# Performance work log

Hardware: AMD Instinct MI355X
Metric: run time of the kernel (lower is better)

## Reference

```python
import jax, jax.numpy as jnp
import numpy as np
from jax import lax

KSIZE = 7
EPS = 1e-10


def _circular_mask(k=KSIZE):
    # faithful to EdgeLoss.cal_mask: inclusive circle, normalized by count
    xs = np.arange(k, dtype=np.float32)
    d2 = (xs[:, None] + 0.5 - k / 2) ** 2 + (xs[None, :] + 0.5 - k / 2) ** 2
    m = (d2 <= ((k - 1) / 2) ** 2).astype(np.float32)
    return jnp.asarray(m / m.sum())


def _gather_logp(prob, target):
    # prob: (B,C,H,W), target: (B,H,W) int -> log prob at target class, (B,1,H,W)
    logpt = jnp.log(prob + EPS)
    return jnp.take_along_axis(logpt, target[:, None, :, :], axis=1)


def _focal0(prob, target):
    # FocalLoss(gamma=0, alpha=None): mean of -log p_t
    return jnp.mean(-_gather_logp(prob, target))


def _dice(prob, target):
    t = target.astype(prob.dtype)          # (B,H,W)
    p = prob[:, 1, :, :]                   # foreground channel
    I = jnp.sum(p * t, axis=(1, 2))
    U = jnp.sum(p + t, axis=(1, 2))
    return 1.0 - jnp.mean(2.0 * I / (U + EPS))


def _edge(prob, target, mask):
    # circular box-filter average of target == unfold+mask sum (zero padding)
    t = target.astype(prob.dtype)[:, None, :, :]  # (B,1,H,W)
    ave = lax.conv_general_dilated(t, mask[None, None, :, :], (1, 1), 'SAME')
    at = jnp.abs(t - ave)                          # edge weight (B,1,H,W)
    lp = _gather_logp(prob, target)                # (B,1,H,W)
    return jnp.mean(-lp * at)


def _calloss(prob, target, sigmas, mask):
    return (_focal0(prob, target) / sigmas[0]
            + _dice(prob, target) / sigmas[1]
            + _edge(prob, target, mask) / sigmas[2])


def setup_inputs() -> dict:
    key = jax.random.key(0)
    k1, k2, k3, k4, k5 = jax.random.split(key, 5)
    N, M, B, C, H, W = 2, 1, 8, 2, 1024, 1024
    predictions = jax.random.normal(k1, (N, B, C, H, W), dtype=jnp.float32)
    Diss = jax.random.uniform(k2, (M, B, C, H, W), dtype=jnp.float32)
    target = jax.random.randint(k3, (B, H, W), 0, 2, dtype=jnp.int32)
    diff = jax.random.normal(k4, (), dtype=jnp.float32)
    sigma = jax.random.uniform(k5, (3,), dtype=jnp.float32, minval=0.5, maxval=1.5)
    return {"predictions": predictions, "Diss": Diss, "target": target,
            "diff": diff, "sigma": sigma}


def reference(predictions, Diss, target, diff, sigma):
    mask = _circular_mask()
    sigmas = sigma * sigma
    loss = jnp.asarray(0.0, dtype=predictions.dtype)
    for i in range(predictions.shape[0]):            # deep-supervision heads
        prob = jax.nn.softmax(predictions[i], axis=1)
        loss = loss + _calloss(prob, target, sigmas, mask)
    for j in range(Diss.shape[0]):                   # already-probabilities
        loss = loss + _calloss(Diss[j], target, sigmas, mask)
    loss = loss + diff                               # len(diff) != 0 branch
    loss = loss + jnp.sum(jnp.log(sigmas)) / 2
    return loss
```

## Files before the change

kernel.cpp:

```cpp
#include <hip/hip_runtime.h>
#include <math.h>

#define BB 8
#define HH 1024
#define WW 1024
#define HW (1024*1024)

#define TW 128
#define TH 16
#define HALO_H (TH+6)
#define TSTRIDE 136
#define NCOPY 32
#define NSLOT 18

__global__ __launch_bounds__(256)
void loss_main(const float* __restrict__ pred,
               const float* __restrict__ diss,
               const int*   __restrict__ target,
               double*      __restrict__ acc)
{
    __shared__ float tile[HALO_H][TSTRIDE];
    __shared__ float h5[HALO_H][TW];
    __shared__ float h7[HALO_H][TW];
    __shared__ float red[4][12];

    const int bx = blockIdx.x;
    const int by = blockIdx.y;
    const int b  = blockIdx.z;
    const int x0 = bx * TW, y0 = by * TH;
    const int tid = threadIdx.x;
    const int txx = tid & 31;
    const int ty  = tid >> 5;

    const int* tgt_b = target + (size_t)b * HW;
    for (int ch = tid; ch < HALO_H * 34; ch += 256) {
        int r = ch / 34;
        int m = ch - r * 34;
        int gy  = y0 - 3 + r;
        int gxb = x0 - 4 + 4 * m;
        float4 v = make_float4(0.f, 0.f, 0.f, 0.f);
        if (gy >= 0 && gy < HH) {
            if (gxb >= 0 && gxb + 3 < WW) {
                const int4 iv = *(const int4*)(tgt_b + (size_t)gy * WW + gxb);
                v.x = (float)iv.x; v.y = (float)iv.y;
                v.z = (float)iv.z; v.w = (float)iv.w;
            } else {
                #pragma unroll
                for (int j = 0; j < 4; ++j) {
                    int gx = gxb + j;
                    ((float*)&v)[j] = (gx >= 0 && gx < WW)
                        ? (float)tgt_b[(size_t)gy * WW + gx] : 0.f;
                }
            }
        }
        *(float4*)&tile[r][4 * m] = v;
    }
    __syncthreads();

    for (int g = tid; g < HALO_H * 32; g += 256) {
        int r  = g >> 5;
        int xg = (g & 31) << 2;
        float4 c0 = *(const float4*)&tile[r][xg];
        float4 c1 = *(const float4*)&tile[r][xg + 4];
        float4 c2 = *(const float4*)&tile[r][xg + 8];
        float s1 = c0.y, s2 = c0.z, s3 = c0.w;
        float s4 = c1.x, s5 = c1.y, s6 = c1.z, s7 = c1.w;
        float s8 = c2.x, s9 = c2.y, s10 = c2.z;
        float4 v5, v7;
        v5.x = s2 + s3 + s4 + s5 + s6;
        v5.y = s3 + s4 + s5 + s6 + s7;
        v5.z = s4 + s5 + s6 + s7 + s8;
        v5.w = s5 + s6 + s7 + s8 + s9;
        v7.x = v5.x + s1 + s7;
        v7.y = v5.y + s2 + s8;
        v7.z = v5.z + s3 + s9;
        v7.w = v5.w + s4 + s10;
        *(float4*)&h5[r][xg] = v5;
        *(float4*)&h7[r][xg] = v7;
    }
    __syncthreads();

    const float* p00 = pred + ((size_t)(0 * BB + b) * 2 + 0) * HW;
    const float* p01 = p00 + HW;
    const float* p10 = pred + ((size_t)(1 * BB + b) * 2 + 0) * HW;
    const float* p11 = p10 + HW;
    const float* q0  = diss + ((size_t)b * 2 + 0) * HW;
    const float* q1  = q0 + HW;

    float sf0=0.f, se0=0.f, si0=0.f, su0=0.f;
    float sf1=0.f, se1=0.f, si1=0.f, su1=0.f;
    float sf2=0.f, se2=0.f, si2=0.f, su2=0.f;

    const int x  = txx * 4;
    const int gx = x0 + x;
    #pragma unroll
    for (int k = 0; k < 2; ++k) {
        const int r  = ty + 8 * k;
        const int gy = y0 + r;
        const size_t off = (size_t)gy * WW + gx;

        float4 t4  = *(const float4*)&tile[r + 3][x + 4];
        float4 top = *(const float4*)&tile[r    ][x + 4];
        float4 bot = *(const float4*)&tile[r + 6][x + 4];
        float4 a1v = *(const float4*)&h5[r + 1][x];
        float4 a2v = *(const float4*)&h5[r + 2][x];
        float4 a3v = *(const float4*)&h7[r + 3][x];
        float4 a4v = *(const float4*)&h5[r + 4][x];
        float4 a5v = *(const float4*)&h5[r + 5][x];

        float4 v00 = *(const float4*)(p00 + off);
        float4 v01 = *(const float4*)(p01 + off);
        float4 v10 = *(const float4*)(p10 + off);
        float4 v11 = *(const float4*)(p11 + off);
        float4 w0  = *(const float4*)(q0  + off);
        float4 w1  = *(const float4*)(q1  + off);

        float4 cnt;
        cnt.x = top.x + a1v.x + a2v.x + a3v.x + a4v.x + a5v.x + bot.x;
        cnt.y = top.y + a1v.y + a2v.y + a3v.y + a4v.y + a5v.y + bot.y;
        cnt.z = top.z + a1v.z + a2v.z + a3v.z + a4v.z + a5v.z + bot.z;
        cnt.w = top.w + a1v.w + a2v.w + a3v.w + a4v.w + a5v.w + bot.w;

        #pragma unroll
        for (int j = 0; j < 4; ++j) {
            const float t  = ((const float*)&t4)[j];
            const float at = fabsf(t - ((const float*)&cnt)[j] * (1.0f / 29.0f));
            {
                float a0 = ((const float*)&v00)[j], a1 = ((const float*)&v01)[j];
                float p1v = __builtin_amdgcn_rcpf(1.0f + __expf(a0 - a1));
                float pt  = (t != 0.0f) ? p1v : 1.0f - p1v;
                float lp  = __logf(pt + 1e-10f);
                sf0 -= lp; se0 -= lp * at; si0 += p1v * t; su0 += p1v + t;
            }
            {
                float a0 = ((const float*)&v10)[j], a1 = ((const float*)&v11)[j];
                float p1v = __builtin_amdgcn_rcpf(1.0f + __expf(a0 - a1));
                float pt  = (t != 0.0f) ? p1v : 1.0f - p1v;
                float lp  = __logf(pt + 1e-10f);
                sf1 -= lp; se1 -= lp * at; si1 += p1v * t; su1 += p1v + t;
            }
            {
                float d0 = ((const float*)&w0)[j], d1 = ((const float*)&w1)[j];
                float pt = (t != 0.0f) ? d1 : d0;
                float lp = __logf(pt + 1e-10f);
                sf2 -= lp; se2 -= lp * at; si2 += d1 * t; su2 += d1 + t;
            }
        }
    }

    float vals[12] = {sf0,se0,si0,su0, sf1,se1,si1,su1, sf2,se2,si2,su2};
    #pragma unroll
    for (int j = 0; j < 12; ++j) {
        float v = vals[j];
        #pragma unroll
        for (int s = 32; s > 0; s >>= 1) v += __shfl_down(v, s, 64);
        vals[j] = v;
    }
    const int wave = tid >> 6;
    const int lane = tid & 63;
    if (lane == 0) {
        #pragma unroll
        for (int j = 0; j < 12; ++j) red[wave][j] = vals[j];
    }
    __syncthreads();
    if (tid < 12) {
        double s = (double)red[0][tid] + (double)red[1][tid]
                 + (double)red[2][tid] + (double)red[3][tid];
        const int img  = tid >> 2;
        const int what = tid & 3;
        int slot;
        if      (what == 0) slot = 0;
        else if (what == 1) slot = 1;
        else if (what == 2) slot = 2 + b;
        else                slot = 10 + b;
        const int copy = (by * 8 + bx) & (NCOPY - 1);
        unsafeAtomicAdd(acc + ((size_t)(img * NSLOT + slot) * NCOPY + copy), s);
    }
}

__global__ __launch_bounds__(256)
void finalize_kernel(const double* __restrict__ acc,
                     const float*  __restrict__ diff,
                     const float*  __restrict__ sigma,
                     float*        __restrict__ out)
{
    __shared__ double ssum[54];
    const int t = threadIdx.x;
    if (t < 216) {
        const int slot_lin = t >> 2;
        const int part     = t & 3;
        const double* p = acc + (size_t)slot_lin * NCOPY + part * 8;
        double s = 0.0;
        #pragma unroll
        for (int j = 0; j < 8; ++j) s += p[j];
        s += __shfl_down(s, 1, 64);
        s += __shfl_down(s, 2, 64);
        if (part == 0) ssum[slot_lin] = s;
    }
    __syncthreads();
    if (t == 0) {
        const double sig0 = (double)sigma[0] * (double)sigma[0];
        const double sig1 = (double)sigma[1] * (double)sigma[1];
        const double sig2 = (double)sigma[2] * (double)sigma[2];
        const double inv  = 1.0 / (double)((size_t)BB * HW);
        double loss = 0.0;
        for (int i = 0; i < 3; ++i) {
            const double* A = ssum + i * NSLOT;
            double focal = A[0] * inv;
            double edge  = A[1] * inv;
            double dsum  = 0.0;
            for (int b = 0; b < BB; ++b)
                dsum += 2.0 * A[2 + b] / (A[10 + b] + 1e-10);
            double dice = 1.0 - dsum / (double)BB;
            loss += focal / sig0 + dice / sig1 + edge / sig2;
        }
        loss += (double)diff[0];
        loss += 0.5 * (log(sig0) + log(sig1) + log(sig2));
        out[0] = (float)loss;
    }
}

extern "C" void kernel_launch(void* const* d_in, const int* in_sizes, int n_in,
                              void* d_out, int out_size, void* d_ws, size_t ws_size,
                              hipStream_t stream)
{
    const float* pred   = (const float*)d_in[0];
    const float* diss   = (const float*)d_in[1];
    const int*   target = (const int*)  d_in[2];
    const float* diff   = (const float*)d_in[3];
    const float* sigma  = (const float*)d_in[4];
    double* acc = (double*)d_ws;

    hipMemsetAsync(d_ws, 0, (size_t)3 * NSLOT * NCOPY * sizeof(double), stream);

    dim3 grid(WW / TW, HH / TH, BB);
    loss_main<<<grid, 256, 0, stream>>>(pred, diss, target, acc);
    finalize_kernel<<<1, 256, 0, stream>>>(acc, diff, sigma, (float*)d_out);
}
```

Baseline: 270.6 us.

## Pack target tile into bytes and compute box sums with SWAR integer adds

Stores the target halo tile and horizontal partial sums as packed 8-bit lanes instead of floats. The 5- and 7-wide horizontal sums and the vertical accumulation then run as SIMD-within-a-register integer adds. This cuts shared memory roughly fourfold, allowing a higher occupancy hint (launch bounds of 8 blocks), and reduces LDS traffic and ALU work. It relies on the box count fitting in 8 bits (at most 29) and on target values being 0/1, and adds byte extraction and int-to-float conversions per pixel.

```diff
diff --git a/kernel.cpp b/kernel.cpp
--- a/kernel.cpp
+++ b/kernel.cpp
@@ -13,15 +13,15 @@
 #define NCOPY 32
 #define NSLOT 18
 
-__global__ __launch_bounds__(256)
+__global__ __launch_bounds__(256, 8)
 void loss_main(const float* __restrict__ pred,
                const float* __restrict__ diss,
                const int*   __restrict__ target,
                double*      __restrict__ acc)
 {
-    __shared__ float tile[HALO_H][TSTRIDE];
-    __shared__ float h5[HALO_H][TW];
-    __shared__ float h7[HALO_H][TW];
+    __shared__ __align__(16) unsigned char tile[HALO_H][TSTRIDE];
+    __shared__ __align__(16) unsigned char h5[HALO_H][TW];
+    __shared__ __align__(16) unsigned char h7[HALO_H][TW];
     __shared__ float red[4][12];
 
     const int bx = blockIdx.x;
@@ -38,45 +38,43 @@
         int m = ch - r * 34;
         int gy  = y0 - 3 + r;
         int gxb = x0 - 4 + 4 * m;
-        float4 v = make_float4(0.f, 0.f, 0.f, 0.f);
+        unsigned v = 0u;
         if (gy >= 0 && gy < HH) {
             if (gxb >= 0 && gxb + 3 < WW) {
                 const int4 iv = *(const int4*)(tgt_b + (size_t)gy * WW + gxb);
-                v.x = (float)iv.x; v.y = (float)iv.y;
-                v.z = (float)iv.z; v.w = (float)iv.w;
+                v = (unsigned)(iv.x & 0xff)
+                  | ((unsigned)(iv.y & 0xff) << 8)
+                  | ((unsigned)(iv.z & 0xff) << 16)
+                  | ((unsigned)(iv.w & 0xff) << 24);
             } else {
                 #pragma unroll
                 for (int j = 0; j < 4; ++j) {
                     int gx = gxb + j;
-                    ((float*)&v)[j] = (gx >= 0 && gx < WW)
-                        ? (float)tgt_b[(size_t)gy * WW + gx] : 0.f;
+                    if (gx >= 0 && gx < WW)
+                        v |= (unsigned)(tgt_b[(size_t)gy * WW + gx] & 0xff) << (8 * j);
                 }
             }
         }
-        *(float4*)&tile[r][4 * m] = v;
+        *(unsigned*)&tile[r][4 * m] = v;
     }
     __syncthreads();
 
     for (int g = tid; g < HALO_H * 32; g += 256) {
         int r  = g >> 5;
         int xg = (g & 31) << 2;
-        float4 c0 = *(const float4*)&tile[r][xg];
-        float4 c1 = *(const float4*)&tile[r][xg + 4];
-        float4 c2 = *(const float4*)&tile[r][xg + 8];
-        float s1 = c0.y, s2 = c0.z, s3 = c0.w;
-        float s4 = c1.x, s5 = c1.y, s6 = c1.z, s7 = c1.w;
-        float s8 = c2.x, s9 = c2.y, s10 = c2.z;
-        float4 v5, v7;
-        v5.x = s2 + s3 + s4 + s5 + s6;
-        v5.y = s3 + s4 + s5 + s6 + s7;
-        v5.z = s4 + s5 + s6 + s7 + s8;
-        v5.w = s5 + s6 + s7 + s8 + s9;
-        v7.x = v5.x + s1 + s7;
-        v7.y = v5.y + s2 + s8;
-        v7.z = v5.z + s3 + s9;
-        v7.w = v5.w + s4 + s10;
-        *(float4*)&h5[r][xg] = v5;
-        *(float4*)&h7[r][xg] = v7;
+        unsigned c0 = *(const unsigned*)&tile[r][xg];
+        unsigned c1 = *(const unsigned*)&tile[r][xg + 4];
+        unsigned c2 = *(const unsigned*)&tile[r][xg + 8];
+        unsigned A1 = (c0 >> 8)  | (c1 << 24);
+        unsigned A2 = (c0 >> 16) | (c1 << 16);
+        unsigned A3 = (c0 >> 24) | (c1 << 8);
+        unsigned A5 = (c1 >> 8)  | (c2 << 24);
+        unsigned A6 = (c1 >> 16) | (c2 << 16);
+        unsigned A7 = (c1 >> 24) | (c2 << 8);
+        unsigned v5 = A2 + A3 + c1 + A5 + A6;
+        unsigned v7 = v5 + A1 + A7;
+        *(unsigned*)&h5[r][xg] = v5;
+        *(unsigned*)&h7[r][xg] = v7;
     }
     __syncthreads();
 
@@ -99,14 +97,14 @@
         const int gy = y0 + r;
         const size_t off = (size_t)gy * WW + gx;
 
-        float4 t4  = *(const float4*)&tile[r + 3][x + 4];
-        float4 top = *(const float4*)&tile[r    ][x + 4];
-        float4 bot = *(const float4*)&tile[r + 6][x + 4];
-        float4 a1v = *(const float4*)&h5[r + 1][x];
-        float4 a2v = *(const float4*)&h5[r + 2][x];
-        float4 a3v = *(const float4*)&h7[r + 3][x];
-        float4 a4v = *(const float4*)&h5[r + 4][x];
-        float4 a5v = *(const float4*)&h5[r + 5][x];
+        const unsigned t4   = *(const unsigned*)&tile[r + 3][x + 4];
+        const unsigned cnt4 = *(const unsigned*)&tile[r    ][x + 4]
+                            + *(const unsigned*)&tile[r + 6][x + 4]
+                            + *(const unsigned*)&h5[r + 1][x]
+                            + *(const unsigned*)&h5[r + 2][x]
+                            + *(const unsigned*)&h7[r + 3][x]
+                            + *(const unsigned*)&h5[r + 4][x]
+                            + *(const unsigned*)&h5[r + 5][x];
 
         float4 v00 = *(const float4*)(p00 + off);
         float4 v01 = *(const float4*)(p01 + off);
@@ -115,33 +113,28 @@
         float4 w0  = *(const float4*)(q0  + off);
         float4 w1  = *(const float4*)(q1  + off);
 
-        float4 cnt;
-        cnt.x = top.x + a1v.x + a2v.x + a3v.x + a4v.x + a5v.x + bot.x;
-        cnt.y = top.y + a1v.y + a2v.y + a3v.y + a4v.y + a5v.y + bot.y;
-        cnt.z = top.z + a1v.z + a2v.z + a3v.z + a4v.z + a5v.z + bot.z;
-        cnt.w = top.w + a1v.w + a2v.w + a3v.w + a4v.w + a5v.w + bot.w;
-
         #pragma unroll
         for (int j = 0; j < 4; ++j) {
-            const float t  = ((const float*)&t4)[j];
-            const float at = fabsf(t - ((const float*)&cnt)[j] * (1.0f / 29.0f));
+            const unsigned tb = (t4 >> (8 * j)) & 0xffu;
+            const float t  = (float)tb;
+            const float at = fabsf(t - (float)((cnt4 >> (8 * j)) & 0xffu) * (1.0f / 29.0f));
             {
                 float a0 = ((const float*)&v00)[j], a1 = ((const float*)&v01)[j];
                 float p1v = __builtin_amdgcn_rcpf(1.0f + __expf(a0 - a1));
-                float pt  = (t != 0.0f) ? p1v : 1.0f - p1v;
+                float pt  = (tb != 0u) ? p1v : 1.0f - p1v;
                 float lp  = __logf(pt + 1e-10f);
                 sf0 -= lp; se0 -= lp * at; si0 += p1v * t; su0 += p1v + t;
             }
             {
                 float a0 = ((const float*)&v10)[j], a1 = ((const float*)&v11)[j];
                 float p1v = __builtin_amdgcn_rcpf(1.0f + __expf(a0 - a1));
-                float pt  = (t != 0.0f) ? p1v : 1.0f - p1v;
+                float pt  = (tb != 0u) ? p1v : 1.0f - p1v;
                 float lp  = __logf(pt + 1e-10f);
                 sf1 -= lp; se1 -= lp * at; si1 += p1v * t; su1 += p1v + t;
             }
             {
                 float d0 = ((const float*)&w0)[j], d1 = ((const float*)&w1)[j];
-                float pt = (t != 0.0f) ? d1 : d0;
+                float pt = (tb != 0u) ? d1 : d0;
                 float lp = __logf(pt + 1e-10f);
                 sf2 -= lp; se2 -= lp * at; si2 += d1 * t; su2 += d1 + t;
             }
```

After: 271.4 us. No clear change (+0.3%).
